# Optimization experiments

Hardware: AMD Instinct MI355X
Metric: run time of the kernel (lower is better)

Reference implementation:

```python
import jax, jax.numpy as jnp
import numpy as np
import math

E = 1024      # embed_dim
H = 16        # num_heads
HD = E // H   # head_dim
NBITS = 8


def fake_quant(x, n_bits=NBITS):
    """Symmetric per-tensor fake quantize with STE (clamp/round/dequant)."""
    qmax = 2.0 ** (n_bits - 1) - 1.0
    qmin = -(2.0 ** (n_bits - 1))
    scale = jnp.maximum(jnp.max(jnp.abs(x)) / qmax, 1e-8)
    xq = jnp.round(jnp.clip(x / scale, qmin, qmax)) * scale
    return x + jax.lax.stop_gradient(xq - x)


def setup_inputs() -> dict:
    key = jax.random.key(0)
    ks = jax.random.split(key, 7)
    L, B = 2048, 2
    query = jax.random.normal(ks[0], (L, B, E), dtype=jnp.float32)
    k_in = jax.random.normal(ks[1], (L, B, E), dtype=jnp.float32)
    v_in = jax.random.normal(ks[2], (L, B, E), dtype=jnp.float32)
    in_w = jax.random.normal(ks[3], (3 * E, E), dtype=jnp.float32) * (1.0 / math.sqrt(E))
    in_b = jax.random.normal(ks[4], (3 * E,), dtype=jnp.float32) * 0.01
    out_w = jax.random.normal(ks[5], (E, E), dtype=jnp.float32) * (1.0 / math.sqrt(E))
    out_b = jax.random.normal(ks[6], (E,), dtype=jnp.float32) * 0.01
    return {"query": query, "key": k_in, "value": v_in,
            "in_w": in_w, "in_b": in_b, "out_w": out_w, "out_b": out_b}


def reference(query, key, value, in_w, in_b, out_w, out_b):
    # NOTE: the original module ignores `key`/`value` (pure self-attention on query),
    # and its attn / softmax fake-quant lines are dead statements (results discarded).
    L, B, _ = query.shape
    Wi = fake_quant(in_w)
    Wo = fake_quant(out_w)
    # input projection: [L,B,3E]
    X = jnp.einsum('lbe,fe->lbf', query, Wi) + in_b
    X = fake_quant(X)
    Q, K, V = jnp.split(X, 3, axis=-1)  # each [L,B,E]
    # [L, B*H, HD] -> [B*H, L, HD]
    q = Q.reshape(L, B * H, HD).transpose(1, 0, 2)
    k = K.reshape(L, B * H, HD).transpose(1, 0, 2)
    v = V.reshape(L, B * H, HD).transpose(1, 0, 2)
    q = q / math.sqrt(HD)
    q = fake_quant(q)
    attn = jnp.einsum('bqd,bkd->bqk', q, k)          # [B*H, L, L]
    attn = jax.nn.softmax(attn, axis=-1)
    heads = jnp.einsum('bqk,bkd->bqd', attn, v)      # [B*H, L, HD]
    heads = fake_quant(heads)
    # [B*H, L, HD] -> [L, B*H, HD] -> [L*B, E]
    heads_r = heads.transpose(1, 0, 2).reshape(L * B, E)
    y = heads_r @ Wo.T + out_b
    y = y.reshape(L, B, E)
    return fake_quant(y)
```

## Files before the change

kernel.cpp:

```cpp
#include <hip/hip_runtime.h>
#include <math.h>

#define L_SEQ 2048
#define BATCH 2
#define EMB 1024
#define NH 16
#define HDIM 64
#define F3 3072
#define NROWS 4096

typedef __bf16 bf16_t;
typedef short s16x8 __attribute__((ext_vector_type(8)));
typedef float f32x4 __attribute__((ext_vector_type(4)));

#define MFMA16(a, b, c) __builtin_amdgcn_mfma_f32_16x16x32_bf16(a, b, c, 0, 0, 0)


__device__ __forceinline__ float u2f(unsigned u) { return __uint_as_float(u); }

__device__ __forceinline__ unsigned short bfb(bf16_t x) {
  union { bf16_t b; unsigned short u; } c; c.b = x; return c.u;
}

__device__ __forceinline__ void gload16(const bf16_t* g, bf16_t* lds) {
  __builtin_amdgcn_global_load_lds((const __attribute__((address_space(1))) void*)g,
                                   (__attribute__((address_space(3))) void*)lds, 16, 0, 0);
}

__device__ __forceinline__ void blockmax_commit(float m, unsigned* slot) {
  #pragma unroll
  for (int o = 1; o < 64; o <<= 1) m = fmaxf(m, __shfl_xor(m, o));
  __shared__ float sm_[4];
  if ((threadIdx.x & 63) == 0) sm_[threadIdx.x >> 6] = m;
  __syncthreads();
  if (threadIdx.x == 0) {
    float mm = fmaxf(fmaxf(sm_[0], sm_[1]), fmaxf(sm_[2], sm_[3]));
    atomicMax(slot, __float_as_uint(mm));
  }
}

__global__ __launch_bounds__(256) void wabsmax_k(const float* __restrict__ wi,
                                                 const float* __restrict__ wo,
                                                 unsigned* __restrict__ slots) {
  float m0 = 0.0f, m1 = 0.0f;
  const int n0 = F3 * EMB / 4, n1 = EMB * EMB / 4;
  for (int i = blockIdx.x * blockDim.x + threadIdx.x; i < n0; i += gridDim.x * blockDim.x) {
    float4 v = ((const float4*)wi)[i];
    m0 = fmaxf(m0, fmaxf(fmaxf(fabsf(v.x), fabsf(v.y)), fmaxf(fabsf(v.z), fabsf(v.w))));
  }
  for (int i = blockIdx.x * blockDim.x + threadIdx.x; i < n1; i += gridDim.x * blockDim.x) {
    float4 v = ((const float4*)wo)[i];
    m1 = fmaxf(m1, fmaxf(fmaxf(fabsf(v.x), fabsf(v.y)), fmaxf(fabsf(v.z), fabsf(v.w))));
  }
  blockmax_commit(m0, slots + 0);
  blockmax_commit(m1, slots + 1);
}

__global__ __launch_bounds__(256) void prep_k(const float* __restrict__ wi,
                                              const float* __restrict__ wo,
                                              const float* __restrict__ query,
                                              bf16_t* __restrict__ Wi_int,
                                              bf16_t* __restrict__ Wo_int,
                                              bf16_t* __restrict__ q_hi,
                                              bf16_t* __restrict__ q_lo,
                                              const unsigned* __restrict__ slots) {
  float s0 = fmaxf(u2f(slots[0]) / 127.0f, 1e-8f);
  float s1 = fmaxf(u2f(slots[1]) / 127.0f, 1e-8f);
  const int n0 = F3 * EMB / 4, n1 = EMB * EMB / 4, n2 = NROWS * EMB / 4;
  for (int i = blockIdx.x * blockDim.x + threadIdx.x; i < n0; i += gridDim.x * blockDim.x) {
    float4 v = ((const float4*)wi)[i];
    bf16_t o[4];
    o[0] = (bf16_t)rintf(fminf(fmaxf(v.x / s0, -128.0f), 127.0f));
    o[1] = (bf16_t)rintf(fminf(fmaxf(v.y / s0, -128.0f), 127.0f));
    o[2] = (bf16_t)rintf(fminf(fmaxf(v.z / s0, -128.0f), 127.0f));
    o[3] = (bf16_t)rintf(fminf(fmaxf(v.w / s0, -128.0f), 127.0f));
    *(uint2*)&Wi_int[(size_t)i * 4] = *(uint2*)o;
  }
  for (int i = blockIdx.x * blockDim.x + threadIdx.x; i < n1; i += gridDim.x * blockDim.x) {
    float4 v = ((const float4*)wo)[i];
    bf16_t o[4];
    o[0] = (bf16_t)rintf(fminf(fmaxf(v.x / s1, -128.0f), 127.0f));
    o[1] = (bf16_t)rintf(fminf(fmaxf(v.y / s1, -128.0f), 127.0f));
    o[2] = (bf16_t)rintf(fminf(fmaxf(v.z / s1, -128.0f), 127.0f));
    o[3] = (bf16_t)rintf(fminf(fmaxf(v.w / s1, -128.0f), 127.0f));
    *(uint2*)&Wo_int[(size_t)i * 4] = *(uint2*)o;
  }
  for (int i = blockIdx.x * blockDim.x + threadIdx.x; i < n2; i += gridDim.x * blockDim.x) {
    float4 v = ((const float4*)query)[i];
    bf16_t h[4], l[4];
    float vv[4] = {v.x, v.y, v.z, v.w};
    #pragma unroll
    for (int j = 0; j < 4; ++j) {
      h[j] = (bf16_t)vv[j];
      l[j] = (bf16_t)(vv[j] - (float)h[j]);
    }
    *(uint2*)&q_hi[(size_t)i * 4] = *(uint2*)h;
    *(uint2*)&q_lo[(size_t)i * 4] = *(uint2*)l;
  }
}

__global__ __launch_bounds__(256) void quantX_k(const float* __restrict__ x,
                                                bf16_t* __restrict__ y,
                                                unsigned* __restrict__ slots) {
  float s = fmaxf(u2f(slots[2]) / 127.0f, 1e-8f);
  float qm = 0.0f;
  const int n8 = NROWS * 256;
  for (int i = blockIdx.x * blockDim.x + threadIdx.x; i < n8; i += gridDim.x * blockDim.x) {
    int row = i >> 8, ch = i & 255;
    const float* px = x + (size_t)row * F3 + ch * 8;
    float4 v0 = *(const float4*)px;
    float4 v1 = *(const float4*)(px + 4);
    float vv[8] = {v0.x, v0.y, v0.z, v0.w, v1.x, v1.y, v1.z, v1.w};
    bf16_t o[8];
    float lm = 0.0f;
    #pragma unroll
    for (int j = 0; j < 8; ++j) {
      float q = rintf(fminf(fmaxf(vv[j] / s, -128.0f), 127.0f));
      o[j] = (bf16_t)q;
      lm = fmaxf(lm, fabsf(q));
    }
    if (ch < 128) qm = fmaxf(qm, lm);
    *(uint4*)&y[(size_t)row * F3 + ch * 8] = *(uint4*)o;
  }
  blockmax_commit(qm, slots + 3);
}

__global__ __launch_bounds__(256) void quant_k(float* __restrict__ x, int n4,
                                               const unsigned* __restrict__ slots, int sloti) {
  float s = fmaxf(u2f(slots[sloti]) / 127.0f, 1e-8f);
  float4* x4 = (float4*)x;
  for (int i = blockIdx.x * blockDim.x + threadIdx.x; i < n4; i += gridDim.x * blockDim.x) {
    float4 v = x4[i];
    v.x = rintf(fminf(fmaxf(v.x / s, -128.0f), 127.0f)) * s;
    v.y = rintf(fminf(fmaxf(v.y / s, -128.0f), 127.0f)) * s;
    v.z = rintf(fminf(fmaxf(v.z / s, -128.0f), 127.0f)) * s;
    v.w = rintf(fminf(fmaxf(v.w / s, -128.0f), 127.0f)) * s;
    x4[i] = v;
  }
}

__global__ __launch_bounds__(256) void quantf_k(const float* __restrict__ x,
                                                bf16_t* __restrict__ y, int n4,
                                                const unsigned* __restrict__ slots, int sloti) {
  float s = fmaxf(u2f(slots[sloti]) / 127.0f, 1e-8f);
  const float4* x4 = (const float4*)x;
  for (int i = blockIdx.x * blockDim.x + threadIdx.x; i < n4; i += gridDim.x * blockDim.x) {
    float4 v = x4[i];
    bf16_t o[4];
    o[0] = (bf16_t)rintf(fminf(fmaxf(v.x / s, -128.0f), 127.0f));
    o[1] = (bf16_t)rintf(fminf(fmaxf(v.y / s, -128.0f), 127.0f));
    o[2] = (bf16_t)rintf(fminf(fmaxf(v.z / s, -128.0f), 127.0f));
    o[3] = (bf16_t)rintf(fminf(fmaxf(v.w / s, -128.0f), 127.0f));
    *(uint2*)&y[(size_t)i * 4] = *(uint2*)o;
  }
}

__global__ __launch_bounds__(256) void vtrans_k(const float* __restrict__ X,
                                                bf16_t* __restrict__ Vt,
                                                const unsigned* __restrict__ slots) {
  float s = fmaxf(u2f(slots[2]) / 127.0f, 1e-8f);
  __shared__ __align__(16) bf16_t tile[64][72];
  int tt = blockIdx.x, bh = blockIdx.y;
  int b = bh >> 4, h = bh & 15;
  int t = threadIdx.x;
  #pragma unroll
  for (int i = 0; i < 2; ++i) {
    int s_ = t + i * 256;
    int tok = s_ >> 3, seg = s_ & 7;
    const float* px = X + ((size_t)(tt * 64 + tok) * BATCH + b) * F3 + 2 * EMB + h * HDIM + seg * 8;
    float4 v0 = *(const float4*)px;
    float4 v1 = *(const float4*)(px + 4);
    float vv[8] = {v0.x, v0.y, v0.z, v0.w, v1.x, v1.y, v1.z, v1.w};
    bf16_t o[8];
    #pragma unroll
    for (int j = 0; j < 8; ++j)
      o[j] = (bf16_t)rintf(fminf(fmaxf(vv[j] / s, -128.0f), 127.0f));
    int segs = seg ^ (tok >> 3);
    *(uint4*)&tile[tok][segs * 8] = *(uint4*)o;
  }
  __syncthreads();
  #pragma unroll
  for (int i = 0; i < 2; ++i) {
    int s_ = t + i * 256;
    int d = s_ >> 3, tseg = s_ & 7;
    bf16_t o[8];
    #pragma unroll
    for (int e = 0; e < 8; ++e) {
      int tok = tseg * 8 + e;
      o[e] = tile[tok][(((d >> 3) ^ (tok >> 3)) << 3) | (d & 7)];
    }
    *(uint4*)&Vt[((size_t)bh * HDIM + d) * L_SEQ + tt * 64 + tseg * 8] = *(uint4*)o;
  }
}

template <int NPARTS>
__global__ __launch_bounds__(256) void gemm_bt_mfma_k(const bf16_t* __restrict__ A0,
                                                      const bf16_t* __restrict__ A1,
                                                      const bf16_t* __restrict__ Bm,
                                                      const float* __restrict__ bias,
                                                      float* __restrict__ C,
                                                      int M, int N, int K,
                                                      unsigned* __restrict__ slots,
                                                      int sa, int sb, int smax) {
  __shared__ __align__(16) bf16_t sbuf[2][NPARTS + 1][128][32];
  int t = threadIdx.x;
  int w = t >> 6, l = t & 63, c15 = l & 15, g = l >> 4;
  int wr = w >> 1, wc = w & 1;
  int nx = gridDim.x;
  int fid = blockIdx.y * nx + blockIdx.x;
  int qq = (nx * gridDim.y) >> 3;
  int swz = (fid & 7) * qq + (fid >> 3);
  int bm = (swz / nx) * 128, bn = (swz % nx) * 128;
  f32x4 acc[4][4] = {};

  auto stage = [&](int bf, int k0) {
    #pragma unroll
    for (int i = 0; i < 2; ++i) {
      int c = i * 256 + t;
      int row = c >> 2, sg = c & 3;
      int wb = (i * 256 + w * 64) * 8;
      gload16(&A0[(size_t)(bm + row) * K + k0 + sg * 8], &sbuf[bf][0][0][0] + wb);
      if (NPARTS == 2)
        gload16(&A1[(size_t)(bm + row) * K + k0 + sg * 8], &sbuf[bf][1][0][0] + wb);
      gload16(&Bm[(size_t)(bn + row) * K + k0 + sg * 8], &sbuf[bf][NPARTS][0][0] + wb);
    }
  };

  stage(0, 0);
  __syncthreads();
  const int nk = K / 32;
  for (int kt = 0; kt < nk; ++kt) {
    int cur = kt & 1;
    if (kt + 1 < nk) stage(cur ^ 1, (kt + 1) * 32);
    s16x8 af[NPARTS][4], bf_[4];
    #pragma unroll
    for (int rt = 0; rt < 4; ++rt) {
      af[0][rt] = *(const s16x8*)&sbuf[cur][0][wr * 64 + rt * 16 + c15][g * 8];
      if (NPARTS == 2) af[1][rt] = *(const s16x8*)&sbuf[cur][1][wr * 64 + rt * 16 + c15][g * 8];
    }
    #pragma unroll
    for (int ct = 0; ct < 4; ++ct)
      bf_[ct] = *(const s16x8*)&sbuf[cur][NPARTS][wc * 64 + ct * 16 + c15][g * 8];
    __builtin_amdgcn_s_setprio(1);
    #pragma unroll
    for (int rt = 0; rt < 4; ++rt)
      #pragma unroll
      for (int ct = 0; ct < 4; ++ct) {
        acc[rt][ct] = MFMA16(af[0][rt], bf_[ct], acc[rt][ct]);
        if (NPARTS == 2) acc[rt][ct] = MFMA16(af[1][rt], bf_[ct], acc[rt][ct]);
      }
    __builtin_amdgcn_s_setprio(0);
    __syncthreads();
  }

  float s = 1.0f;
  if (sa >= 0) s *= fmaxf(u2f(slots[sa]) / 127.0f, 1e-8f);
  if (sb >= 0) s *= fmaxf(u2f(slots[sb]) / 127.0f, 1e-8f);
  float vmax = 0.0f;
  #pragma unroll
  for (int rt = 0; rt < 4; ++rt)
    #pragma unroll
    for (int r = 0; r < 4; ++r) {
      int row = bm + wr * 64 + rt * 16 + 4 * g + r;
      #pragma unroll
      for (int ct = 0; ct < 4; ++ct) {
        int col = bn + wc * 64 + ct * 16 + c15;
        float o = acc[rt][ct][r] * s + bias[col];
        vmax = fmaxf(vmax, fabsf(o));
        C[(size_t)row * N + col] = o;
      }
    }
  if (smax >= 0) blockmax_commit(vmax, slots + smax);
}

__global__ __launch_bounds__(256) void attn_mfma_k(const bf16_t* __restrict__ X,
                                                   const bf16_t* __restrict__ Vt,
                                                   float* __restrict__ heads,
                                                   unsigned* __restrict__ slots) {
  int qb = blockIdx.x, bh = blockIdx.y;
  int b = bh >> 4, h = bh & 15;
  int t = threadIdx.x;
  int w = t >> 6, l = t & 63, c15 = l & 15, g = l >> 4;

  float s_x = fmaxf(u2f(slots[2]) / 127.0f, 1e-8f);
  float s_q = fmaxf((u2f(slots[3]) * s_x) * 0.125f / 127.0f, 1e-8f);
  const float LOG2E = 1.4426950408889634f;
  float qsl2 = s_q * s_x * LOG2E;

  __shared__ __align__(16) union SmKV {
    struct { bf16_t Ks[64][72]; bf16_t Vs[64][72]; } kv;
    float Ot[4][16][69];
  } sm;
  __shared__ __align__(16) bf16_t Pl[4][16][136];

  int qrow = qb * 64 + w * 16 + c15;
  const bf16_t* qbase = X + ((size_t)qrow * BATCH + b) * F3 + h * HDIM;
  s16x8 qf0, qf1;
  {
    bf16_t qt[8];
    #pragma unroll
    for (int half = 0; half < 2; ++half) {
      *(uint4*)qt = *(const uint4*)(qbase + half * 32 + g * 8);
      #pragma unroll
      for (int j = 0; j < 8; ++j) {
        float q = ((float)qt[j] * s_x) * 0.125f;
        qt[j] = (bf16_t)rintf(fminf(fmaxf(q / s_q, -128.0f), 127.0f));
      }
      if (half == 0) qf0 = *(s16x8*)qt; else qf1 = *(s16x8*)qt;
    }
  }

  int r0 = t >> 3, sg0 = t & 7;
  const size_t tokstride = (size_t)BATCH * F3;
  const bf16_t* kp = X + (size_t)r0 * tokstride + (size_t)b * F3 + EMB + h * HDIM + sg0 * 8;
  const bf16_t* vbase = Vt + (size_t)bh * HDIM * L_SEQ;
  const bf16_t* vp = vbase + (size_t)r0 * L_SEQ + sg0 * 8;

  uint4 gk0, gk1, gv0, gv1;
  auto loadg = [&](int kt) {
    size_t ko = (size_t)kt * 64 * tokstride;
    gk0 = *(const uint4*)(kp + ko);
    gk1 = *(const uint4*)(kp + ko + 32 * tokstride);
    int vo = kt * 64;
    gv0 = *(const uint4*)(vp + vo);
    gv1 = *(const uint4*)(vp + vo + 32 * L_SEQ);
  };
  auto write_lds = [&]() {
    *(uint4*)&sm.kv.Ks[r0][sg0 * 8] = gk0;
    *(uint4*)&sm.kv.Ks[r0 + 32][sg0 * 8] = gk1;
    *(uint4*)&sm.kv.Vs[r0][sg0 * 8] = gv0;
    *(uint4*)&sm.kv.Vs[r0 + 32][sg0 * 8] = gv1;
  };

  f32x4 acc_o[4] = {};
  float m_prev = -INFINITY, lsum = 0.0f;

  loadg(0);
  write_lds();
  __syncthreads();

  const int NT = L_SEQ / 64;
  for (int kt = 0; kt < NT; ++kt) {
    if (kt + 1 < NT) loadg(kt + 1);

    f32x4 accs[4] = {};
    __builtin_amdgcn_s_setprio(1);
    #pragma unroll
    for (int ct = 0; ct < 4; ++ct) {
      s16x8 kf0 = *(const s16x8*)&sm.kv.Ks[ct * 16 + c15][g * 8];
      s16x8 kf1 = *(const s16x8*)&sm.kv.Ks[ct * 16 + c15][32 + g * 8];
      accs[ct] = MFMA16(kf0, qf0, accs[ct]);
      accs[ct] = MFMA16(kf1, qf1, accs[ct]);
    }
    __builtin_amdgcn_s_setprio(0);

    float pm = accs[0][0];
    #pragma unroll
    for (int ct = 0; ct < 4; ++ct)
      #pragma unroll
      for (int r = 0; r < 4; ++r) pm = fmaxf(pm, accs[ct][r]);
    pm = fmaxf(pm, __shfl_xor(pm, 16));
    pm = fmaxf(pm, __shfl_xor(pm, 32));
    float mnew = fmaxf(m_prev, pm);
    float f_ = __builtin_amdgcn_exp2f((m_prev - mnew) * qsl2);
    float mq = mnew * qsl2;
    float ps = 0.0f;
    #pragma unroll
    for (int ct = 0; ct < 4; ++ct) {
      float p[4];
      #pragma unroll
      for (int r = 0; r < 4; ++r) p[r] = __builtin_amdgcn_exp2f(fmaf(accs[ct][r], qsl2, -mq));
      ps += (p[0] + p[1]) + (p[2] + p[3]);
      bf16_t h_[4], l_[4];
      #pragma unroll
      for (int r = 0; r < 4; ++r) { h_[r] = (bf16_t)p[r]; l_[r] = (bf16_t)(p[r] - (float)h_[r]); }
      uint2 hw, lw;
      hw.x = (unsigned)bfb(h_[0]) | ((unsigned)bfb(h_[1]) << 16);
      hw.y = (unsigned)bfb(h_[2]) | ((unsigned)bfb(h_[3]) << 16);
      lw.x = (unsigned)bfb(l_[0]) | ((unsigned)bfb(l_[1]) << 16);
      lw.y = (unsigned)bfb(l_[2]) | ((unsigned)bfb(l_[3]) << 16);
      *(uint2*)&Pl[w][c15][ct * 16 + g * 4] = hw;
      *(uint2*)&Pl[w][c15][64 + ct * 16 + g * 4] = lw;
    }
    lsum = lsum * f_ + ps;
    m_prev = mnew;

    if (!__all(f_ == 1.0f)) {
      #pragma unroll
      for (int dt = 0; dt < 4; ++dt)
        #pragma unroll
        for (int r = 0; r < 4; ++r) acc_o[dt][r] *= f_;
    }

    s16x8 pf_h0 = *(const s16x8*)&Pl[w][c15][g * 8];
    s16x8 pf_h1 = *(const s16x8*)&Pl[w][c15][32 + g * 8];
    s16x8 pf_l0 = *(const s16x8*)&Pl[w][c15][64 + g * 8];
    s16x8 pf_l1 = *(const s16x8*)&Pl[w][c15][96 + g * 8];
    __builtin_amdgcn_s_setprio(1);
    #pragma unroll
    for (int dt = 0; dt < 4; ++dt) {
      s16x8 vf0 = *(const s16x8*)&sm.kv.Vs[dt * 16 + c15][g * 8];
      s16x8 vf1 = *(const s16x8*)&sm.kv.Vs[dt * 16 + c15][32 + g * 8];
      acc_o[dt] = MFMA16(vf0, pf_h0, acc_o[dt]);
      acc_o[dt] = MFMA16(vf1, pf_h1, acc_o[dt]);
      acc_o[dt] = MFMA16(vf0, pf_l0, acc_o[dt]);
      acc_o[dt] = MFMA16(vf1, pf_l1, acc_o[dt]);
    }
    __builtin_amdgcn_s_setprio(0);

    __syncthreads();
    if (kt + 1 < NT) write_lds();
    __syncthreads();
  }

  lsum += __shfl_xor(lsum, 16);
  lsum += __shfl_xor(lsum, 32);
  float inv = s_x / lsum;

  float hm = 0.0f;
  #pragma unroll
  for (int dt = 0; dt < 4; ++dt)
    #pragma unroll
    for (int r = 0; r < 4; ++r) {
      float o = acc_o[dt][r] * inv;
      hm = fmaxf(hm, fabsf(o));
      sm.Ot[w][c15][dt * 16 + 4 * g + r] = o;
    }
  int ql = l >> 2, cs = l & 3;
  #pragma unroll
  for (int j = 0; j < 4; ++j) {
    int cch = cs + 4 * j;
    float4 v = *(const float4*)&sm.Ot[w][ql][cch * 4];
    int row = qb * 64 + w * 16 + ql;
    *(float4*)&heads[((size_t)row * BATCH + b) * EMB + h * HDIM + cch * 4] = v;
  }
  blockmax_commit(hm, slots + 4);
}

extern "C" void kernel_launch(void* const* d_in, const int* in_sizes, int n_in,
                              void* d_out, int out_size, void* d_ws, size_t ws_size,
                              hipStream_t stream) {
  (void)in_sizes; (void)n_in; (void)out_size; (void)ws_size;
  const float* query = (const float*)d_in[0];
  const float* in_w  = (const float*)d_in[3];
  const float* in_b  = (const float*)d_in[4];
  const float* out_w = (const float*)d_in[5];
  const float* out_b = (const float*)d_in[6];
  float* out = (float*)d_out;

  unsigned* slots = (unsigned*)d_ws;
  char* p = (char*)d_ws + 256;
  bf16_t* q_hi   = (bf16_t*)p;                  p += (size_t)NROWS * EMB * 2;
  bf16_t* q_lo   = (bf16_t*)p;                  p += (size_t)NROWS * EMB * 2;
  bf16_t* Wi_int = (bf16_t*)p;                  p += (size_t)F3 * EMB * 2;
  bf16_t* Wo_int = (bf16_t*)p;                  p += (size_t)EMB * EMB * 2;
  float*  X_f32  = (float*)p;                   p += (size_t)NROWS * F3 * 4;
  bf16_t* X_int  = (bf16_t*)p;
  bf16_t* Vt     = q_hi;
  bf16_t* heads_int = (bf16_t*)X_f32;
  float*  heads_f32 = out;

  hipMemsetAsync(d_ws, 0, 256, stream);

  dim3 b256(256);
  wabsmax_k<<<768, b256, 0, stream>>>(in_w, out_w, slots);
  prep_k<<<1024, b256, 0, stream>>>(in_w, out_w, query, Wi_int, Wo_int, q_hi, q_lo, slots);

  gemm_bt_mfma_k<2><<<dim3(F3 / 128, NROWS / 128), b256, 0, stream>>>(
      q_hi, q_lo, Wi_int, in_b, X_f32, NROWS, F3, EMB, slots, -1, 0, 2);

  quantX_k<<<2048, b256, 0, stream>>>(X_f32, X_int, slots);

  vtrans_k<<<dim3(L_SEQ / 64, BATCH * NH), b256, 0, stream>>>(X_f32, Vt, slots);

  attn_mfma_k<<<dim3(L_SEQ / 64, BATCH * NH), b256, 0, stream>>>(X_int, Vt, heads_f32, slots);

  quantf_k<<<1024, b256, 0, stream>>>(heads_f32, heads_int, NROWS * EMB / 4, slots, 4);

  gemm_bt_mfma_k<1><<<dim3(EMB / 128, NROWS / 128), b256, 0, stream>>>(
      heads_int, nullptr, Wo_int, out_b, out, NROWS, EMB, EMB, slots, 4, 1, 5);

  quant_k<<<1024, b256, 0, stream>>>(out, NROWS * EMB / 4, slots, 5);
}
```

Baseline: 257.3 us.

## Double-buffer K/V via async global-to-LDS loads with XOR swizzle, keep P in registers

Replaces the register-staged K/V tile loads with direct global_load_lds into a double-buffered, XOR-swizzled LDS layout. This removes one barrier per iteration and the register round trip. The P probabilities (hi/lo bf16 split) are now packed straight into MFMA operand registers instead of going through an LDS scratch buffer. K rows are permuted on load (kap mapping) so that the C-layout of the QK MFMA output matches the B-operand layout needed for PV. The correctness of that permutation is subtle and it doubles the LDS used for K/V.

Result: faster. 247.7 us (-3.7%).

```diff
diff --git a/kernel.cpp b/kernel.cpp
--- a/kernel.cpp
+++ b/kernel.cpp
@@ -17,10 +17,6 @@
 
 
 __device__ __forceinline__ float u2f(unsigned u) { return __uint_as_float(u); }
-
-__device__ __forceinline__ unsigned short bfb(bf16_t x) {
-  union { bf16_t b; unsigned short u; } c; c.b = x; return c.u;
-}
 
 __device__ __forceinline__ void gload16(const bf16_t* g, bf16_t* lds) {
   __builtin_amdgcn_global_load_lds((const __attribute__((address_space(1))) void*)g,
@@ -288,10 +284,9 @@
   float qsl2 = s_q * s_x * LOG2E;
 
   __shared__ __align__(16) union SmKV {
-    struct { bf16_t Ks[64][72]; bf16_t Vs[64][72]; } kv;
+    struct { bf16_t K[2][64][64]; bf16_t V[2][64][64]; } kv;
     float Ot[4][16][69];
   } sm;
-  __shared__ __align__(16) bf16_t Pl[4][16][136];
 
   int qrow = qb * 64 + w * 16 + c15;
   const bf16_t* qbase = X + ((size_t)qrow * BATCH + b) * F3 + h * HDIM;
@@ -310,45 +305,47 @@
     }
   }
 
-  int r0 = t >> 3, sg0 = t & 7;
   const size_t tokstride = (size_t)BATCH * F3;
-  const bf16_t* kp = X + (size_t)r0 * tokstride + (size_t)b * F3 + EMB + h * HDIM + sg0 * 8;
+  const bf16_t* kbase = X + (size_t)b * F3 + EMB + h * HDIM;
   const bf16_t* vbase = Vt + (size_t)bh * HDIM * L_SEQ;
-  const bf16_t* vp = vbase + (size_t)r0 * L_SEQ + sg0 * 8;
-
-  uint4 gk0, gk1, gv0, gv1;
-  auto loadg = [&](int kt) {
-    size_t ko = (size_t)kt * 64 * tokstride;
-    gk0 = *(const uint4*)(kp + ko);
-    gk1 = *(const uint4*)(kp + ko + 32 * tokstride);
-    int vo = kt * 64;
-    gv0 = *(const uint4*)(vp + vo);
-    gv1 = *(const uint4*)(vp + vo + 32 * L_SEQ);
-  };
-  auto write_lds = [&]() {
-    *(uint4*)&sm.kv.Ks[r0][sg0 * 8] = gk0;
-    *(uint4*)&sm.kv.Ks[r0 + 32][sg0 * 8] = gk1;
-    *(uint4*)&sm.kv.Vs[r0][sg0 * 8] = gv0;
-    *(uint4*)&sm.kv.Vs[r0 + 32][sg0 * 8] = gv1;
+
+  auto stage = [&](int buf, int kt) {
+    #pragma unroll
+    for (int i = 0; i < 2; ++i) {
+      int c = i * 256 + t;
+      int a = c >> 3, blk = c & 7;
+      int kap = (a & 0x20) | ((a & 0x10) >> 2) | ((a & 0x0C) << 1) | (a & 3);
+      gload16(kbase + (size_t)(kt * 64 + kap) * tokstride + (blk ^ (a & 7)) * 8,
+              &sm.kv.K[buf][0][0] + (i * 256 + w * 64) * 8);
+    }
+    #pragma unroll
+    for (int i = 0; i < 2; ++i) {
+      int c = i * 256 + t;
+      int d = c >> 3, blk = c & 7;
+      gload16(vbase + (size_t)d * L_SEQ + kt * 64 + (blk ^ (d & 7)) * 8,
+              &sm.kv.V[buf][0][0] + (i * 256 + w * 64) * 8);
+    }
   };
 
   f32x4 acc_o[4] = {};
   float m_prev = -INFINITY, lsum = 0.0f;
-
-  loadg(0);
-  write_lds();
+  int sw = c15 & 7;
+
+  stage(0, 0);
   __syncthreads();
 
   const int NT = L_SEQ / 64;
+  int cur = 0;
   for (int kt = 0; kt < NT; ++kt) {
-    if (kt + 1 < NT) loadg(kt + 1);
+    if (kt + 1 < NT) stage(cur ^ 1, kt + 1);
 
     f32x4 accs[4] = {};
     __builtin_amdgcn_s_setprio(1);
     #pragma unroll
     for (int ct = 0; ct < 4; ++ct) {
-      s16x8 kf0 = *(const s16x8*)&sm.kv.Ks[ct * 16 + c15][g * 8];
-      s16x8 kf1 = *(const s16x8*)&sm.kv.Ks[ct * 16 + c15][32 + g * 8];
+      const bf16_t* krow = &sm.kv.K[cur][ct * 16 + c15][0];
+      s16x8 kf0 = *(const s16x8*)(krow + (g ^ sw) * 8);
+      s16x8 kf1 = *(const s16x8*)(krow + ((g | 4) ^ sw) * 8);
       accs[ct] = MFMA16(kf0, qf0, accs[ct]);
       accs[ct] = MFMA16(kf1, qf1, accs[ct]);
     }
@@ -365,22 +362,19 @@
     float f_ = __builtin_amdgcn_exp2f((m_prev - mnew) * qsl2);
     float mq = mnew * qsl2;
     float ps = 0.0f;
+    bf16_t hh[2][8], ll[2][8];
     #pragma unroll
     for (int ct = 0; ct < 4; ++ct) {
       float p[4];
       #pragma unroll
       for (int r = 0; r < 4; ++r) p[r] = __builtin_amdgcn_exp2f(fmaf(accs[ct][r], qsl2, -mq));
       ps += (p[0] + p[1]) + (p[2] + p[3]);
-      bf16_t h_[4], l_[4];
-      #pragma unroll
-      for (int r = 0; r < 4; ++r) { h_[r] = (bf16_t)p[r]; l_[r] = (bf16_t)(p[r] - (float)h_[r]); }
-      uint2 hw, lw;
-      hw.x = (unsigned)bfb(h_[0]) | ((unsigned)bfb(h_[1]) << 16);
-      hw.y = (unsigned)bfb(h_[2]) | ((unsigned)bfb(h_[3]) << 16);
-      lw.x = (unsigned)bfb(l_[0]) | ((unsigned)bfb(l_[1]) << 16);
-      lw.y = (unsigned)bfb(l_[2]) | ((unsigned)bfb(l_[3]) << 16);
-      *(uint2*)&Pl[w][c15][ct * 16 + g * 4] = hw;
-      *(uint2*)&Pl[w][c15][64 + ct * 16 + g * 4] = lw;
+      #pragma unroll
+      for (int r = 0; r < 4; ++r) {
+        bf16_t hi = (bf16_t)p[r];
+        hh[ct >> 1][(ct & 1) * 4 + r] = hi;
+        ll[ct >> 1][(ct & 1) * 4 + r] = (bf16_t)(p[r] - (float)hi);
+      }
     }
     lsum = lsum * f_ + ps;
     m_prev = mnew;
@@ -392,25 +386,23 @@
         for (int r = 0; r < 4; ++r) acc_o[dt][r] *= f_;
     }
 
-    s16x8 pf_h0 = *(const s16x8*)&Pl[w][c15][g * 8];
-    s16x8 pf_h1 = *(const s16x8*)&Pl[w][c15][32 + g * 8];
-    s16x8 pf_l0 = *(const s16x8*)&Pl[w][c15][64 + g * 8];
-    s16x8 pf_l1 = *(const s16x8*)&Pl[w][c15][96 + g * 8];
+    s16x8 pfh0 = *(s16x8*)hh[0], pfh1 = *(s16x8*)hh[1];
+    s16x8 pfl0 = *(s16x8*)ll[0], pfl1 = *(s16x8*)ll[1];
     __builtin_amdgcn_s_setprio(1);
     #pragma unroll
     for (int dt = 0; dt < 4; ++dt) {
-      s16x8 vf0 = *(const s16x8*)&sm.kv.Vs[dt * 16 + c15][g * 8];
-      s16x8 vf1 = *(const s16x8*)&sm.kv.Vs[dt * 16 + c15][32 + g * 8];
-      acc_o[dt] = MFMA16(vf0, pf_h0, acc_o[dt]);
-      acc_o[dt] = MFMA16(vf1, pf_h1, acc_o[dt]);
-      acc_o[dt] = MFMA16(vf0, pf_l0, acc_o[dt]);
-      acc_o[dt] = MFMA16(vf1, pf_l1, acc_o[dt]);
+      const bf16_t* vrow = &sm.kv.V[cur][dt * 16 + c15][0];
+      s16x8 vf0 = *(const s16x8*)(vrow + (g ^ sw) * 8);
+      s16x8 vf1 = *(const s16x8*)(vrow + ((g | 4) ^ sw) * 8);
+      acc_o[dt] = MFMA16(vf0, pfh0, acc_o[dt]);
+      acc_o[dt] = MFMA16(vf1, pfh1, acc_o[dt]);
+      acc_o[dt] = MFMA16(vf0, pfl0, acc_o[dt]);
+      acc_o[dt] = MFMA16(vf1, pfl1, acc_o[dt]);
     }
     __builtin_amdgcn_s_setprio(0);
 
     __syncthreads();
-    if (kt + 1 < NT) write_lds();
-    __syncthreads();
+    cur ^= 1;
   }
 
   lsum += __shfl_xor(lsum, 16);
```
